# Optimization experiments

Measured on AMD Instinct MI355X. Metric: run time of the kernel, lower is better.

Reference implementation:

```python
import jax, jax.numpy as jnp
import numpy as np
import math

B, C, D, NH, L, DFF = 128, 112, 512, 8, 13, 1920
DK = D // NH  # 64
_pos = np.arange(64)
_ranks, _files = _pos // 8, _pos % 8
RIDX = np.clip(_ranks[:, None] - _ranks[None, :], -7, 7) + 7  # [64,64] rel-rank bucket
FIDX = np.clip(_files[:, None] - _files[None, :], -7, 7) + 7  # [64,64] rel-file bucket
DIAG = _ranks + _files        # [64] in [0,14]
ADIAG = _ranks - _files + 7   # [64] in [0,14]


def _ln(x, g, b):
    m = jnp.mean(x, -1, keepdims=True)
    v = jnp.mean((x - m) ** 2, -1, keepdims=True)
    return (x - m) * jax.lax.rsqrt(v + 1e-5) * g + b


def setup_inputs() -> dict:
    key = jax.random.key(0)
    ks = iter(jax.random.split(key, 40))
    nrm = lambda *s: jax.random.normal(next(ks), s, jnp.float32) * 0.02
    return dict(
        x=jax.random.normal(next(ks), (B, C, 8, 8), jnp.float32),
        conv_w=nrm(C, D), conv_b=jnp.zeros(D),
        cls_token=nrm(1, 1, D),
        abs_pos=nrm(1, 64, D),
        file_emb=nrm(8, D), rank_emb=nrm(8, D),
        diag_emb=nrm(15, D), anti_diag_emb=nrm(15, D),
        ln1_g=jnp.ones((L, D)), ln1_b=jnp.zeros((L, D)),
        wq=nrm(L, D, D), bq=jnp.zeros((L, D)),
        wk=nrm(L, D, D), bk=jnp.zeros((L, D)),
        wv=nrm(L, D, D), bv=jnp.zeros((L, D)),
        wo=nrm(L, D, D), bo=jnp.zeros((L, D)),
        rel_bias=nrm(L, 15, 15, NH),
        ln2_g=jnp.ones((L, D)), ln2_b=jnp.zeros((L, D)),
        w_ff1=nrm(L, D, 2 * DFF), b_ff1=jnp.zeros((L, 2 * DFF)),
        w_ff2=nrm(L, DFF, D), b_ff2=jnp.zeros((L, D)),
        out_g=jnp.ones(D), out_b=jnp.zeros(D),
        vw1=nrm(D, D // 2), vb1=jnp.zeros(D // 2),
        vw2=nrm(D // 2, 128), vb2=jnp.zeros(128),
        vw3=nrm(128, 3), vb3=jnp.zeros(3),
        pw=nrm(D, 72), pb=jnp.zeros(72),
    )


def reference(x, conv_w, conv_b, cls_token, abs_pos, file_emb, rank_emb, diag_emb, anti_diag_emb,
              ln1_g, ln1_b, wq, bq, wk, bk, wv, bv, wo, bo, rel_bias, ln2_g, ln2_b,
              w_ff1, b_ff1, w_ff2, b_ff2, out_g, out_b,
              vw1, vb1, vw2, vb2, vw3, vb3, pw, pb):
    Bc = x.shape[0]
    # 1x1 conv == channel-wise linear; flatten spatial (row-major: s = rank*8 + file)
    tok = jnp.einsum('bcs,cd->bsd', x.reshape(Bc, C, 64), conv_w) + conv_b  # [B,64,D]
    pos = abs_pos + file_emb[_files] + rank_emb[_ranks] + diag_emb[DIAG] + anti_diag_emb[ADIAG]
    tok = tok + pos
    h = jnp.concatenate([jnp.broadcast_to(cls_token, (Bc, 1, D)), tok], axis=1)  # [B,65,D]
    scale = 1.0 / math.sqrt(DK)

    def block(hx, p):
        g1, b1, Wq, Bq, Wk, Bk, Wv, Bv, Wo, Bo, rb, g2, b2, W1, B1, W2, B2 = p
        n = _ln(hx, g1, b1)
        q = (n @ Wq + Bq).reshape(Bc, 65, NH, DK).transpose(0, 2, 1, 3)
        k = (n @ Wk + Bk).reshape(Bc, 65, NH, DK).transpose(0, 2, 1, 3)
        v = (n @ Wv + Bv).reshape(Bc, 65, NH, DK).transpose(0, 2, 1, 3)
        # gather relative-position bias [64,64,H] -> [H,65,65] with zero row/col for CLS
        bias = jnp.pad(jnp.transpose(rb[RIDX, FIDX], (2, 0, 1)), ((0, 0), (1, 0), (1, 0)))
        scores = jnp.einsum('bhqd,bhkd->bhqk', q, k) * scale + bias[None]
        a = jax.nn.softmax(scores, axis=-1)
        ctx = jnp.einsum('bhqk,bhkd->bhqd', a, v).transpose(0, 2, 1, 3).reshape(Bc, 65, D)
        hx = hx + ctx @ Wo + Bo
        n2 = _ln(hx, g2, b2)
        u = n2 @ W1 + B1
        u1, u2 = jnp.split(u, 2, axis=-1)
        hx = hx + (jax.nn.gelu(u1, approximate=False) * u2) @ W2 + B2
        return hx, None

    params = (ln1_g, ln1_b, wq, bq, wk, bk, wv, bv, wo, bo, rel_bias,
              ln2_g, ln2_b, w_ff1, b_ff1, w_ff2, b_ff2)
    h, _ = jax.lax.scan(block, h, params)
    h = _ln(h, out_g, out_b)
    cls = h[:, 0]
    v1 = jax.nn.gelu(cls @ vw1 + vb1, approximate=False)
    v2 = jax.nn.gelu(v1 @ vw2 + vb2, approximate=False)
    value = v2 @ vw3 + vb3                 # WDL logits [B,3]
    policy = (h[:, 1:] @ pw + pb).reshape(Bc, -1)  # [B, 64*72]
    return policy, value
```

## Files before the change

### kernel.cpp

```cpp
#include <hip/hip_runtime.h>
#include <stdint.h>

#define NLAYER 13
#define DMODEL 512
#define SEQ    65
#define BATCH  128
#define MROWS  (BATCH*SEQ)
#define NHEAD  8
#define DFFH   1920
#define MTILES 65
#define MBAND  9

typedef __bf16 bf16x8 __attribute__((ext_vector_type(8)));
typedef float  f32x4  __attribute__((ext_vector_type(4)));

__device__ __forceinline__ float bf2f(unsigned short u) {
    union { unsigned int i; float f; } c; c.i = ((unsigned int)u) << 16; return c.f;
}
__device__ __forceinline__ unsigned short f2bf(float f) {
    union { float f; unsigned int i; } c; c.f = f;
    unsigned int u = c.i;
    u += 0x7fffu + ((u >> 16) & 1u);
    return (unsigned short)(u >> 16);
}
__device__ __forceinline__ float gelu_exact(float x) {
    return 0.5f * x * (1.0f + erff(x * 0.70710678118654752f));
}

__global__ __launch_bounds__(256) void transpose_f32_bf16(
    const float* __restrict__ src, unsigned short* __restrict__ dst,
    int R, int C, int Cpad, long srcLS, long dstLS, int rowOff)
{
    __shared__ float tile[32][33];
    int l  = blockIdx.z;
    int c0 = blockIdx.x * 32, r0 = blockIdx.y * 32;
    const float* s = src + (long)l * srcLS;
    unsigned short* d = dst + (long)l * dstLS;
    int tx = threadIdx.x, ty = threadIdx.y;
#pragma unroll
    for (int k = 0; k < 4; k++) {
        int r = r0 + ty + 8*k, c = c0 + tx;
        float v = (r < R && c < C) ? s[(long)r * C + c] : 0.0f;
        tile[ty + 8*k][tx] = v;
    }
    __syncthreads();
#pragma unroll
    for (int k = 0; k < 4; k++) {
        int c = c0 + ty + 8*k, r = r0 + tx;
        if (c < Cpad && r < R)
            d[(long)(rowOff + c) * R + r] = f2bf(tile[tx][ty + 8*k]);
    }
}

__global__ __launch_bounds__(256) void stack_bias_kernel(
    const float* __restrict__ bq, const float* __restrict__ bk,
    const float* __restrict__ bv, float* __restrict__ bqkv)
{
    int idx = blockIdx.x * 256 + threadIdx.x;
    if (idx >= NLAYER * 1536) return;
    int l = idx / 1536, r = idx - l * 1536;
    float v;
    if (r < 512)       v = bq[l*512 + r];
    else if (r < 1024) v = bk[l*512 + r - 512];
    else               v = bv[l*512 + r - 1024];
    bqkv[idx] = v;
}

__global__ __launch_bounds__(256) void embed_kernel(
    const float* __restrict__ x, const float* __restrict__ conv_w,
    const float* __restrict__ conv_b, const float* __restrict__ cls_tok,
    const float* __restrict__ abs_pos, const float* __restrict__ file_emb,
    const float* __restrict__ rank_emb, const float* __restrict__ diag_emb,
    const float* __restrict__ adiag_emb, float* __restrict__ h)
{
    int b = blockIdx.y, sg = blockIdx.x, t = threadIdx.x;
    if (sg == 8) {
        for (int d = t; d < 512; d += 256)
            h[(long)b * SEQ * 512 + d] = cls_tok[d];
        return;
    }
    __shared__ float xs[112][8];
    for (int idx = t; idx < 112*8; idx += 256) {
        int c = idx >> 3, j = idx & 7;
        xs[c][j] = x[((long)b*112 + c)*64 + sg*8 + j];
    }
    __syncthreads();
    int d0 = t, d1 = t + 256;
    float acc0[8] = {}, acc1[8] = {};
    for (int c = 0; c < 112; c++) {
        float w0 = conv_w[c*512 + d0], w1 = conv_w[c*512 + d1];
#pragma unroll
        for (int j = 0; j < 8; j++) { acc0[j] += xs[c][j]*w0; acc1[j] += xs[c][j]*w1; }
    }
#pragma unroll
    for (int j = 0; j < 8; j++) {
        int sq = sg*8 + j, r = sq >> 3, f = sq & 7;
        long row = ((long)b * SEQ + 1 + sq) * 512;
        h[row + d0] = acc0[j] + conv_b[d0] + abs_pos[sq*512+d0] + file_emb[f*512+d0]
                    + rank_emb[r*512+d0] + diag_emb[(r+f)*512+d0] + adiag_emb[(r-f+7)*512+d0];
        h[row + d1] = acc1[j] + conv_b[d1] + abs_pos[sq*512+d1] + file_emb[f*512+d1]
                    + rank_emb[r*512+d1] + diag_emb[(r+f)*512+d1] + adiag_emb[(r-f+7)*512+d1];
    }
}

__global__ __launch_bounds__(256) void ln_kernel(
    const float* __restrict__ hx, const float* __restrict__ g,
    const float* __restrict__ bb, unsigned short* __restrict__ o)
{
    int row  = blockIdx.x * 4 + (threadIdx.x >> 6);
    int lane = threadIdx.x & 63;
    const float4* xr = (const float4*)(hx + (long)row * 512);
    float4 v0 = xr[lane], v1 = xr[lane + 64];
    float s  = v0.x+v0.y+v0.z+v0.w + v1.x+v1.y+v1.z+v1.w;
    float s2 = v0.x*v0.x+v0.y*v0.y+v0.z*v0.z+v0.w*v0.w
             + v1.x*v1.x+v1.y*v1.y+v1.z*v1.z+v1.w*v1.w;
    for (int off = 32; off; off >>= 1) { s += __shfl_xor(s, off); s2 += __shfl_xor(s2, off); }
    float mean = s * (1.0f/512.0f);
    float var  = s2 * (1.0f/512.0f) - mean*mean;
    float rs   = rsqrtf(var + 1e-5f);
    const float4* gr = (const float4*)g; const float4* br = (const float4*)bb;
    float4 g0 = gr[lane], g1 = gr[lane+64], b0 = br[lane], b1 = br[lane+64];
    ushort4 o0, o1;
    o0.x = f2bf((v0.x-mean)*rs*g0.x + b0.x);
    o0.y = f2bf((v0.y-mean)*rs*g0.y + b0.y);
    o0.z = f2bf((v0.z-mean)*rs*g0.z + b0.z);
    o0.w = f2bf((v0.w-mean)*rs*g0.w + b0.w);
    o1.x = f2bf((v1.x-mean)*rs*g1.x + b1.x);
    o1.y = f2bf((v1.y-mean)*rs*g1.y + b1.y);
    o1.z = f2bf((v1.z-mean)*rs*g1.z + b1.z);
    o1.w = f2bf((v1.w-mean)*rs*g1.w + b1.w);
    ushort4* orow = (ushort4*)(o + (long)row * 512);
    orow[lane] = o0; orow[lane + 64] = o1;
}

template<int MODE>
__global__ __launch_bounds__(256) void gemm128(
    const unsigned short* __restrict__ A, const unsigned short* __restrict__ Bt,
    const float* __restrict__ bias, const float* __restrict__ res,
    void* __restrict__ out, int K, int ldo, int nT)
{
    __shared__ __attribute__((aligned(16))) unsigned short As[128*32];
    __shared__ __attribute__((aligned(16))) unsigned short Bs[128*32];
    int id = blockIdx.x;
    int xcd = id & 7, jj = id >> 3;
    int bn  = jj % nT;
    int mt  = xcd * MBAND + jj / nT;
    if (mt >= MTILES) return;
    int m0 = mt * 128;
    int tid = threadIdx.x;
    int lane = tid & 63, w = tid >> 6;
    int quad = lane >> 4, col = lane & 15;

    int srow = tid >> 2;
    int sc8  = (tid & 3) * 8;

    int br0, br1;
    if (MODE == 2) {
        br0 = bn*64 + srow;
        br1 = 1920 + bn*64 + srow;
    } else {
        br0 = bn*128 + srow;
        br1 = bn*128 + srow + 64;
    }
    const unsigned short* Arow0 = A + (long)(m0 + srow) * K + sc8;
    const unsigned short* Arow1 = A + (long)(m0 + srow + 64) * K + sc8;
    const unsigned short* Brow0 = Bt + (long)br0 * K + sc8;
    const unsigned short* Brow1 = Bt + (long)br1 * K + sc8;

    f32x4 acc[2][8] = {};

    int4 ca0 = *(const int4*)(Arow0);
    int4 ca1 = *(const int4*)(Arow1);
    int4 cb0 = *(const int4*)(Brow0);
    int4 cb1 = *(const int4*)(Brow1);

    for (int k0 = 0; k0 < K; k0 += 32) {
        __syncthreads();
        *(int4*)(&As[srow*32 + sc8])        = ca0;
        *(int4*)(&As[(srow+64)*32 + sc8])   = ca1;
        *(int4*)(&Bs[srow*32 + sc8])        = cb0;
        *(int4*)(&Bs[(srow+64)*32 + sc8])   = cb1;
        __syncthreads();
        int kn = k0 + 32;
        if (kn < K) {
            ca0 = *(const int4*)(Arow0 + kn);
            ca1 = *(const int4*)(Arow1 + kn);
            cb0 = *(const int4*)(Brow0 + kn);
            cb1 = *(const int4*)(Brow1 + kn);
        }
        bf16x8 af[2], bfr[8];
#pragma unroll
        for (int i = 0; i < 2; i++)
            af[i] = *(const bf16x8*)(&As[(w*32 + i*16 + col)*32 + quad*8]);
#pragma unroll
        for (int t = 0; t < 8; t++)
            bfr[t] = *(const bf16x8*)(&Bs[(t*16 + col)*32 + quad*8]);
#pragma unroll
        for (int i = 0; i < 2; i++)
#pragma unroll
            for (int t = 0; t < 8; t++)
                acc[i][t] = __builtin_amdgcn_mfma_f32_16x16x32_bf16(af[i], bfr[t], acc[i][t], 0, 0, 0);
    }

    if (MODE == 2) {
        unsigned short* O = (unsigned short*)out;
        int gn0 = bn * 64;
#pragma unroll
        for (int i = 0; i < 2; i++)
#pragma unroll
        for (int t = 0; t < 4; t++) {
            int c = t*16 + col;
            float b1v = bias[gn0 + c];
            float b2v = bias[1920 + gn0 + c];
#pragma unroll
            for (int r = 0; r < 4; r++) {
                int m = m0 + w*32 + i*16 + quad*4 + r;
                float u1 = acc[i][t][r]   + b1v;
                float u2 = acc[i][t+4][r] + b2v;
                O[(long)m * DFFH + gn0 + c] = f2bf(gelu_exact(u1) * u2);
            }
        }
        return;
    }
    int n0 = bn * 128;
#pragma unroll
    for (int i = 0; i < 2; i++)
#pragma unroll
    for (int t = 0; t < 8; t++) {
        int cg = n0 + t*16 + col;
        float bv = (MODE == 3) ? (cg < 72 ? bias[cg] : 0.0f) : bias[cg];
#pragma unroll
        for (int r = 0; r < 4; r++) {
            int m = m0 + w*32 + i*16 + quad*4 + r;
            float v = acc[i][t][r] + bv;
            if (MODE == 0) {
                ((unsigned short*)out)[(long)m * ldo + cg] = f2bf(v);
            } else if (MODE == 1) {
                ((float*)out)[(long)m * ldo + cg] = res[(long)m * ldo + cg] + v;
            } else {
                if (cg < 72) {
                    int b2 = m / 65, s = m - b2 * 65;
                    if (s > 0)
                        ((float*)out)[(long)b2 * 4608 + (s - 1) * 72 + cg] = v;
                }
            }
        }
    }
}

__global__ __launch_bounds__(256) void attn_mfma_kernel(
    const unsigned short* __restrict__ qkv,
    const float* __restrict__ rel_bias,
    unsigned short* __restrict__ ctx,
    int layer)
{
    constexpr int QS = 72;
    constexpr int VS = 104;
    constexpr int SS = 68;
    constexpr int PS = 104;
    __shared__ __attribute__((aligned(16))) unsigned short Qs[80*QS];
    __shared__ __attribute__((aligned(16))) unsigned short Ks[80*QS];
    __shared__ __attribute__((aligned(16))) unsigned short Vt[64*VS];
    __shared__ __attribute__((aligned(16))) float Sf[65*SS];
    __shared__ __attribute__((aligned(16))) unsigned short Pb[80*PS];
    __shared__ float bias_s[225];

    int h = blockIdx.x, b = blockIdx.y, t = threadIdx.x;
    int lane = t & 63, w = t >> 6;
    int quad = lane >> 4, col = lane & 15;

    for (int i = t; i < 225; i += 256)
        bias_s[i] = rel_bias[((long)layer*225 + i)*8 + h];

    for (int i = t; i < 65*8; i += 256) {
        int s = i >> 3, c8 = (i & 7) * 8;
        const unsigned short* row = qkv + ((long)(b*65+s))*1536 + h*64 + c8;
        int4 qv = *(const int4*)(row);
        int4 kv = *(const int4*)(row + 512);
        int4 vv = *(const int4*)(row + 1024);
        unsigned short qsc[8];
        const unsigned short* qp = (const unsigned short*)&qv;
#pragma unroll
        for (int j = 0; j < 8; j++) qsc[j] = f2bf(bf2f(qp[j]) * 0.125f);
        *(int4*)&Qs[s*QS + c8] = *(const int4*)qsc;
        *(int4*)&Ks[s*QS + c8] = kv;
        const unsigned short* vp = (const unsigned short*)&vv;
#pragma unroll
        for (int j = 0; j < 8; j++) Vt[(c8+j)*VS + s] = vp[j];
    }
    for (int i = t; i < 64*31; i += 256) {
        int d = i / 31, s = 65 + i % 31;
        Vt[d*VS + s] = 0;
    }
    __syncthreads();

    for (int tt = w; tt < 25; tt += 4) {
        int mi = tt / 5, nj = tt % 5;
        f32x4 acc = {};
        bf16x8 a0 = *(const bf16x8*)&Qs[(mi*16+col)*QS + quad*8];
        bf16x8 b0 = *(const bf16x8*)&Ks[(nj*16+col)*QS + quad*8];
        acc = __builtin_amdgcn_mfma_f32_16x16x32_bf16(a0, b0, acc, 0, 0, 0);
        bf16x8 a1 = *(const bf16x8*)&Qs[(mi*16+col)*QS + 32 + quad*8];
        bf16x8 b1 = *(const bf16x8*)&Ks[(nj*16+col)*QS + 32 + quad*8];
        acc = __builtin_amdgcn_mfma_f32_16x16x32_bf16(a1, b1, acc, 0, 0, 0);
#pragma unroll
        for (int r = 0; r < 4; r++) {
            int qi = mi*16 + quad*4 + r, kj = nj*16 + col;
            if (qi < 65 && kj < 65) {
                float v = acc[r];
                if (qi >= 1 && kj >= 1) {
                    int i2 = qi - 1, j2 = kj - 1;
                    int dr = (i2 >> 3) - (j2 >> 3) + 7;
                    int df = (i2 & 7) - (j2 & 7) + 7;
                    v += bias_s[dr*15 + df];
                }
                Sf[qi*SS + kj] = v;
            }
        }
    }
    __syncthreads();

    for (int r = w; r < 65; r += 4) {
        float x0 = Sf[r*SS + lane];
        float x1 = (lane == 0) ? Sf[r*SS + 64] : -1e30f;
        float mx = fmaxf(x0, x1);
        for (int off = 32; off; off >>= 1) mx = fmaxf(mx, __shfl_xor(mx, off));
        float e0 = __expf(x0 - mx);
        float e1 = (lane == 0) ? __expf(x1 - mx) : 0.0f;
        float sm = e0 + e1;
        for (int off = 32; off; off >>= 1) sm += __shfl_xor(sm, off);
        float inv = 1.0f / sm;
        Pb[r*PS + lane] = f2bf(e0 * inv);
        if (lane == 0)  Pb[r*PS + 64] = f2bf(e1 * inv);
        if (lane >= 1 && lane <= 31) Pb[r*PS + 64 + lane] = 0;
    }
    __syncthreads();

    for (int tt = w; tt < 20; tt += 4) {
        int mi = tt >> 2, dj = tt & 3;
        f32x4 acc = {};
#pragma unroll
        for (int ks = 0; ks < 3; ks++) {
            bf16x8 a  = *(const bf16x8*)&Pb[(mi*16+col)*PS + ks*32 + quad*8];
            bf16x8 bb = *(const bf16x8*)&Vt[(dj*16+col)*VS + ks*32 + quad*8];
            acc = __builtin_amdgcn_mfma_f32_16x16x32_bf16(a, bb, acc, 0, 0, 0);
        }
#pragma unroll
        for (int r = 0; r < 4; r++) {
            int qi = mi*16 + quad*4 + r;
            if (qi < 65)
                ctx[((long)(b*65+qi))*512 + h*64 + dj*16 + col] = f2bf(acc[r]);
        }
    }
}

__global__ __launch_bounds__(256) void value_head_kernel(
    const unsigned short* __restrict__ hn,
    const float* __restrict__ vw1, const float* __restrict__ vb1,
    const float* __restrict__ vw2, const float* __restrict__ vb2,
    const float* __restrict__ vw3, const float* __restrict__ vb3,
    float* __restrict__ outv)
{
    int b = blockIdx.x, t = threadIdx.x;
    __shared__ float cls[512], v1[256], v2[128];
    for (int d = t; d < 512; d += 256) cls[d] = bf2f(hn[(long)b * SEQ * 512 + d]);
    __syncthreads();
    {
        float a = vb1[t];
        for (int c = 0; c < 512; c++) a += cls[c] * vw1[c*256 + t];
        v1[t] = gelu_exact(a);
    }
    __syncthreads();
    if (t < 128) {
        float a = vb2[t];
        for (int c = 0; c < 256; c++) a += v1[c] * vw2[c*128 + t];
        v2[t] = gelu_exact(a);
    }
    __syncthreads();
    if (t < 3) {
        float a = vb3[t];
        for (int c = 0; c < 128; c++) a += v2[c] * vw3[c*3 + t];
        outv[b*3 + t] = a;
    }
}

extern "C" void kernel_launch(void* const* d_in, const int* in_sizes, int n_in,
                              void* d_out, int out_size, void* d_ws, size_t ws_size,
                              hipStream_t stream)
{
    (void)in_sizes; (void)n_in; (void)out_size; (void)ws_size;
    const float* x        = (const float*)d_in[0];
    const float* conv_w   = (const float*)d_in[1];
    const float* conv_b   = (const float*)d_in[2];
    const float* cls_tok  = (const float*)d_in[3];
    const float* abs_pos  = (const float*)d_in[4];
    const float* file_emb = (const float*)d_in[5];
    const float* rank_emb = (const float*)d_in[6];
    const float* diag_emb = (const float*)d_in[7];
    const float* adiag    = (const float*)d_in[8];
    const float* ln1_g    = (const float*)d_in[9];
    const float* ln1_b    = (const float*)d_in[10];
    const float* wq       = (const float*)d_in[11];
    const float* bq       = (const float*)d_in[12];
    const float* wk       = (const float*)d_in[13];
    const float* bk       = (const float*)d_in[14];
    const float* wv       = (const float*)d_in[15];
    const float* bv       = (const float*)d_in[16];
    const float* wo       = (const float*)d_in[17];
    const float* bo       = (const float*)d_in[18];
    const float* rel_bias = (const float*)d_in[19];
    const float* ln2_g    = (const float*)d_in[20];
    const float* ln2_b    = (const float*)d_in[21];
    const float* w_ff1    = (const float*)d_in[22];
    const float* b_ff1    = (const float*)d_in[23];
    const float* w_ff2    = (const float*)d_in[24];
    const float* b_ff2    = (const float*)d_in[25];
    const float* out_g    = (const float*)d_in[26];
    const float* out_b    = (const float*)d_in[27];
    const float* vw1      = (const float*)d_in[28];
    const float* vb1      = (const float*)d_in[29];
    const float* vw2      = (const float*)d_in[30];
    const float* vb2      = (const float*)d_in[31];
    const float* vw3      = (const float*)d_in[32];
    const float* vb3      = (const float*)d_in[33];
    const float* pw       = (const float*)d_in[34];
    const float* pb       = (const float*)d_in[35];

    char* p = (char*)d_ws;
    auto alloc = [&](size_t bytes) { void* r = (void*)p; p += (bytes + 255) & ~(size_t)255; return r; };
    unsigned short* qkvT = (unsigned short*)alloc((size_t)NLAYER*1536*512*2);
    unsigned short* woT  = (unsigned short*)alloc((size_t)NLAYER*512*512*2);
    unsigned short* w1T  = (unsigned short*)alloc((size_t)NLAYER*3840*512*2);
    unsigned short* w2T  = (unsigned short*)alloc((size_t)NLAYER*512*1920*2);
    unsigned short* pwT  = (unsigned short*)alloc((size_t)128*512*2);
    float*          bqkv = (float*)alloc((size_t)NLAYER*1536*4);
    float*          h    = (float*)alloc((size_t)MROWS*512*4);
    unsigned short* nbf  = (unsigned short*)alloc((size_t)MROWS*512*2);
    unsigned short* qkvb = (unsigned short*)alloc((size_t)MROWS*1536*2);
    unsigned short* ctxb = (unsigned short*)alloc((size_t)MROWS*512*2);
    unsigned short* gbuf = (unsigned short*)alloc((size_t)MROWS*1920*2);

    dim3 tb(32, 8);
    transpose_f32_bf16<<<dim3(16,16,NLAYER), tb, 0, stream>>>(wq, qkvT, 512, 512, 512, 512L*512, 1536L*512, 0);
    transpose_f32_bf16<<<dim3(16,16,NLAYER), tb, 0, stream>>>(wk, qkvT, 512, 512, 512, 512L*512, 1536L*512, 512);
    transpose_f32_bf16<<<dim3(16,16,NLAYER), tb, 0, stream>>>(wv, qkvT, 512, 512, 512, 512L*512, 1536L*512, 1024);
    transpose_f32_bf16<<<dim3(16,16,NLAYER), tb, 0, stream>>>(wo, woT, 512, 512, 512, 512L*512, 512L*512, 0);
    transpose_f32_bf16<<<dim3(120,16,NLAYER), tb, 0, stream>>>(w_ff1, w1T, 512, 3840, 3840, 512L*3840, 3840L*512, 0);
    transpose_f32_bf16<<<dim3(16,60,NLAYER), tb, 0, stream>>>(w_ff2, w2T, 1920, 512, 512, 1920L*512, 512L*1920, 0);
    transpose_f32_bf16<<<dim3(4,16,1), tb, 0, stream>>>(pw, pwT, 512, 72, 128, 0, 0, 0);
    stack_bias_kernel<<<(NLAYER*1536 + 255)/256, 256, 0, stream>>>(bq, bk, bv, bqkv);

    embed_kernel<<<dim3(9, BATCH), 256, 0, stream>>>(x, conv_w, conv_b, cls_tok, abs_pos,
                                                     file_emb, rank_emb, diag_emb, adiag, h);

    for (int l = 0; l < NLAYER; l++) {
        ln_kernel<<<MROWS/4, 256, 0, stream>>>(h, ln1_g + l*512, ln1_b + l*512, nbf);
        gemm128<0><<<72*12, 256, 0, stream>>>(nbf, qkvT + (size_t)l*1536*512,
                                              bqkv + l*1536, nullptr, qkvb, 512, 1536, 12);
        attn_mfma_kernel<<<dim3(NHEAD, BATCH), 256, 0, stream>>>(qkvb, rel_bias, ctxb, l);
        gemm128<1><<<72*4, 256, 0, stream>>>(ctxb, woT + (size_t)l*512*512,
                                             bo + l*512, h, h, 512, 512, 4);
        ln_kernel<<<MROWS/4, 256, 0, stream>>>(h, ln2_g + l*512, ln2_b + l*512, nbf);
        gemm128<2><<<72*30, 256, 0, stream>>>(nbf, w1T + (size_t)l*3840*512,
                                              b_ff1 + l*3840, nullptr, gbuf, 512, 0, 30);
        gemm128<1><<<72*4, 256, 0, stream>>>(gbuf, w2T + (size_t)l*512*1920,
                                             b_ff2 + l*512, h, h, 1920, 512, 4);
    }

    ln_kernel<<<MROWS/4, 256, 0, stream>>>(h, out_g, out_b, nbf);
    gemm128<3><<<72*1, 256, 0, stream>>>(nbf, pwT, pb, nullptr, (float*)d_out, 512, 0, 1);
    value_head_kernel<<<BATCH, 256, 0, stream>>>(nbf, vw1, vb1, vw2, vb2, vw3, vb3,
                                                 (float*)d_out + (size_t)BATCH*4608);
}
```

Baseline: 2.874 ms.

## Use 2x2 warp tiling, K=64 steps and padded LDS in GEMM kernel

Reorganizes the 128x128 GEMM tile so each of the four waves computes a 64x64 subtile (4x4 MFMA fragments) instead of a 32x128 strip. This cuts LDS fragment reads per MFMA. The K step doubles to 64 with two inner sub-steps, halving the number of barriers. LDS rows are padded to 72 elements to avoid bank conflicts. In exchange it uses more LDS and more prefetch registers per thread, and the B-row interleaving for the gated FFN mode is remapped so u1/u2 columns land in adjacent fragments.

```diff
diff --git a/kernel.cpp b/kernel.cpp
--- a/kernel.cpp
+++ b/kernel.cpp
@@ -139,8 +139,9 @@
     const float* __restrict__ bias, const float* __restrict__ res,
     void* __restrict__ out, int K, int ldo, int nT)
 {
-    __shared__ __attribute__((aligned(16))) unsigned short As[128*32];
-    __shared__ __attribute__((aligned(16))) unsigned short Bs[128*32];
+    constexpr int LDP = 72;
+    __shared__ __attribute__((aligned(16))) unsigned short As[128*LDP];
+    __shared__ __attribute__((aligned(16))) unsigned short Bs[128*LDP];
     int id = blockIdx.x;
     int xcd = id & 7, jj = id >> 3;
     int bn  = jj % nT;
@@ -150,88 +151,93 @@
     int tid = threadIdx.x;
     int lane = tid & 63, w = tid >> 6;
     int quad = lane >> 4, col = lane & 15;
-
-    int srow = tid >> 2;
-    int sc8  = (tid & 3) * 8;
-
-    int br0, br1;
+    int wr = (w & 1) * 64, wc = (w >> 1) * 64;
+
+    int srow = tid >> 1;
+    int sh   = (tid & 1) * 32;
+
+    int brow;
     if (MODE == 2) {
-        br0 = bn*64 + srow;
-        br1 = 1920 + bn*64 + srow;
+        int c = srow >> 5, hb = (srow >> 4) & 1, r16 = srow & 15;
+        brow = (hb ? DFFH : 0) + bn*64 + c*16 + r16;
     } else {
-        br0 = bn*128 + srow;
-        br1 = bn*128 + srow + 64;
-    }
-    const unsigned short* Arow0 = A + (long)(m0 + srow) * K + sc8;
-    const unsigned short* Arow1 = A + (long)(m0 + srow + 64) * K + sc8;
-    const unsigned short* Brow0 = Bt + (long)br0 * K + sc8;
-    const unsigned short* Brow1 = Bt + (long)br1 * K + sc8;
-
-    f32x4 acc[2][8] = {};
-
-    int4 ca0 = *(const int4*)(Arow0);
-    int4 ca1 = *(const int4*)(Arow1);
-    int4 cb0 = *(const int4*)(Brow0);
-    int4 cb1 = *(const int4*)(Brow1);
-
-    for (int k0 = 0; k0 < K; k0 += 32) {
+        brow = bn*128 + srow;
+    }
+    const unsigned short* Arow = A  + (long)(m0 + srow) * K + sh;
+    const unsigned short* Brow = Bt + (long)brow * K + sh;
+    unsigned short* wA = &As[srow*LDP + sh];
+    unsigned short* wB = &Bs[srow*LDP + sh];
+
+    f32x4 acc[4][4] = {};
+    int4 ca[4], cb[4];
+#pragma unroll
+    for (int j = 0; j < 4; j++) {
+        ca[j] = *(const int4*)(Arow + j*8);
+        cb[j] = *(const int4*)(Brow + j*8);
+    }
+
+    for (int k0 = 0; k0 < K; k0 += 64) {
         __syncthreads();
-        *(int4*)(&As[srow*32 + sc8])        = ca0;
-        *(int4*)(&As[(srow+64)*32 + sc8])   = ca1;
-        *(int4*)(&Bs[srow*32 + sc8])        = cb0;
-        *(int4*)(&Bs[(srow+64)*32 + sc8])   = cb1;
+#pragma unroll
+        for (int j = 0; j < 4; j++) {
+            *(int4*)(wA + j*8) = ca[j];
+            *(int4*)(wB + j*8) = cb[j];
+        }
         __syncthreads();
-        int kn = k0 + 32;
+        int kn = k0 + 64;
         if (kn < K) {
-            ca0 = *(const int4*)(Arow0 + kn);
-            ca1 = *(const int4*)(Arow1 + kn);
-            cb0 = *(const int4*)(Brow0 + kn);
-            cb1 = *(const int4*)(Brow1 + kn);
-        }
-        bf16x8 af[2], bfr[8];
-#pragma unroll
-        for (int i = 0; i < 2; i++)
-            af[i] = *(const bf16x8*)(&As[(w*32 + i*16 + col)*32 + quad*8]);
-#pragma unroll
-        for (int t = 0; t < 8; t++)
-            bfr[t] = *(const bf16x8*)(&Bs[(t*16 + col)*32 + quad*8]);
-#pragma unroll
-        for (int i = 0; i < 2; i++)
-#pragma unroll
-            for (int t = 0; t < 8; t++)
-                acc[i][t] = __builtin_amdgcn_mfma_f32_16x16x32_bf16(af[i], bfr[t], acc[i][t], 0, 0, 0);
+#pragma unroll
+            for (int j = 0; j < 4; j++) {
+                ca[j] = *(const int4*)(Arow + kn + j*8);
+                cb[j] = *(const int4*)(Brow + kn + j*8);
+            }
+        }
+#pragma unroll
+        for (int s = 0; s < 2; s++) {
+            bf16x8 af[4], bf[4];
+#pragma unroll
+            for (int i = 0; i < 4; i++)
+                af[i] = *(const bf16x8*)(&As[(wr + i*16 + col)*LDP + s*32 + quad*8]);
+#pragma unroll
+            for (int t = 0; t < 4; t++)
+                bf[t] = *(const bf16x8*)(&Bs[(wc + t*16 + col)*LDP + s*32 + quad*8]);
+#pragma unroll
+            for (int i = 0; i < 4; i++)
+#pragma unroll
+                for (int t = 0; t < 4; t++)
+                    acc[i][t] = __builtin_amdgcn_mfma_f32_16x16x32_bf16(af[i], bf[t], acc[i][t], 0, 0, 0);
+        }
     }
 
     if (MODE == 2) {
         unsigned short* O = (unsigned short*)out;
-        int gn0 = bn * 64;
-#pragma unroll
-        for (int i = 0; i < 2; i++)
-#pragma unroll
-        for (int t = 0; t < 4; t++) {
-            int c = t*16 + col;
-            float b1v = bias[gn0 + c];
-            float b2v = bias[1920 + gn0 + c];
+#pragma unroll
+        for (int i = 0; i < 4; i++)
+#pragma unroll
+        for (int t2 = 0; t2 < 2; t2++) {
+            int ucol = bn*64 + (wc >> 1) + t2*16 + col;
+            float b1v = bias[ucol];
+            float b2v = bias[DFFH + ucol];
 #pragma unroll
             for (int r = 0; r < 4; r++) {
-                int m = m0 + w*32 + i*16 + quad*4 + r;
-                float u1 = acc[i][t][r]   + b1v;
-                float u2 = acc[i][t+4][r] + b2v;
-                O[(long)m * DFFH + gn0 + c] = f2bf(gelu_exact(u1) * u2);
+                int m = m0 + wr + i*16 + quad*4 + r;
+                float u1 = acc[i][2*t2][r]   + b1v;
+                float u2 = acc[i][2*t2+1][r] + b2v;
+                O[(long)m * DFFH + ucol] = f2bf(gelu_exact(u1) * u2);
             }
         }
         return;
     }
     int n0 = bn * 128;
 #pragma unroll
-    for (int i = 0; i < 2; i++)
-#pragma unroll
-    for (int t = 0; t < 8; t++) {
-        int cg = n0 + t*16 + col;
+    for (int i = 0; i < 4; i++)
+#pragma unroll
+    for (int t = 0; t < 4; t++) {
+        int cg = n0 + wc + t*16 + col;
         float bv = (MODE == 3) ? (cg < 72 ? bias[cg] : 0.0f) : bias[cg];
 #pragma unroll
         for (int r = 0; r < 4; r++) {
-            int m = m0 + w*32 + i*16 + quad*4 + r;
+            int m = m0 + wr + i*16 + quad*4 + r;
             float v = acc[i][t][r] + bv;
             if (MODE == 0) {
                 ((unsigned short*)out)[(long)m * ldo + cg] = f2bf(v);
```

After: 7.078 ms. +146.3%, slower.
